# Kernel optimization log

Measured on AMD Instinct MI355X. Metric: run time of the kernel, lower is better.

## Reference

```python
import jax, jax.numpy as jnp
import numpy as np

B, C, H, W = 4, 8, 384, 384
CHANS = 18  # MLP hidden width (module default chans=18)
BAND = 32   # half-width of acquired low-frequency band


def setup_inputs() -> dict:
    key = jax.random.key(0)
    ks = jax.random.split(key, 8)
    acquired_kspace = jax.random.normal(ks[0], (B, C, H, W, 2), jnp.float32)
    acquiring_kspace = jax.random.normal(ks[1], (B, C, H, W, 2), jnp.float32)
    mid = W // 2
    am = np.zeros((B, W), np.float32)
    am[:, mid - BAND:mid + BAND] = 1.0  # acquired center band -> left/right well-defined
    acquired_mask = jnp.asarray(am)
    qm = np.zeros((B, W), np.float32)
    qm[:, ::24] = 1.0  # columns currently being acquired
    acquiring_mask = jnp.asarray(qm)
    CH = C * H
    IN = 2 * CH  # concat(acquiring_features, acquired_features)
    # MLP: Linear(IN,CHANS)+ReLU, Linear(CHANS,CHANS)+ReLU x2, Linear(CHANS,1)+Sigmoid (pools=4 layers)
    W1 = jax.random.normal(ks[2], (CHANS, IN), jnp.float32) * 0.02
    b1 = jnp.zeros((CHANS,), jnp.float32)
    W2 = jax.random.normal(ks[3], (CHANS, CHANS), jnp.float32) * 0.02
    b2 = jnp.zeros((CHANS,), jnp.float32)
    W3 = jax.random.normal(ks[4], (CHANS, CHANS), jnp.float32) * 0.02
    b3 = jnp.zeros((CHANS,), jnp.float32)
    W4 = jax.random.normal(ks[5], (1, CHANS), jnp.float32) * 0.02
    b4 = jnp.zeros((1,), jnp.float32)
    return dict(acquired_kspace=acquired_kspace, acquiring_kspace=acquiring_kspace,
                acquired_mask=acquired_mask, acquiring_mask=acquiring_mask,
                W1=W1, b1=b1, W2=W2, b2=b2, W3=W3, b3=b3, W4=W4, b4=b4)


def reference(acquired_kspace, acquiring_kspace, acquired_mask, acquiring_mask,
              W1, b1, W2, b2, W3, b3, W4, b4):
    cabs = lambda x: jnp.sqrt(jnp.sum(x * x, axis=-1))  # complex magnitude of trailing (re,im)
    # per-column flattened features, row-major over (C,H) like torch.flatten: [B, W, C*H]
    Fq = cabs(acquiring_kspace).transpose(0, 3, 1, 2).reshape(B, W, -1)
    Fa = cabs(acquired_kspace).transpose(0, 3, 1, 2).reshape(B, W, -1)
    CH = Fq.shape[-1]
    # split first linear over the concat([acquiring, acquired]) input
    Pq = Fq @ W1[:, :CH].T   # [B, W_i, CHANS]
    Pa = Fa @ W1[:, CH:].T   # [B, W_c, CHANS]
    h = jax.nn.relu(Pq[:, :, None, :] + Pa[:, None, :, :] + b1)  # [B, W_i, W_c, CHANS]
    h = jax.nn.relu(h @ W2.T + b2)
    h = jax.nn.relu(h @ W3.T + b3)
    out = jax.nn.sigmoid(h @ W4.T + b4)[..., 0]  # [B, W_i, W_c]
    # faithful left/right bounds from acquired_mask (same as torch.nonzero(...)[0][0])
    mid = W // 2
    right = mid + jnp.argmax(acquired_mask[:, mid:] < 1.0, axis=1)              # [B]
    left = jnp.argmax(acquired_mask[:, :mid][:, ::-1] < 1.0, axis=1) + 1        # [B]
    c = jnp.arange(W)
    cmask = (c[None, :] >= left[:, None]) & (c[None, :] < right[:, None])       # [B, W_c]
    denom = (right - left).astype(out.dtype)
    heat = jnp.sum(out * cmask[:, None, :].astype(out.dtype), axis=2) / denom[:, None]
    heat = jnp.where(acquiring_mask > 0, heat, jnp.zeros_like(heat))            # only nonzero acquiring cols
    return jnp.broadcast_to(heat[:, None, :], (B, H, W))  # torch.cat of h copies along dim=1
```

## Files before the change

### kernel.cpp

```cpp
#include <hip/hip_runtime.h>
#include <math.h>
#include <limits.h>

#define kB 4
#define kC 8
#define kH 384
#define kW 384
#define kCH (kC * kH)
#define kIN (2 * kCH)
#define kNC 18
#define kMID (kW / 2)

#define NCH 8
#define RPC (kCH / NCH)
#define NGRP 48
#define kN (kB * kW * kNC)

#define E18(M) M(0) M(1) M(2) M(3) M(4) M(5) M(6) M(7) M(8) M(9) M(10) M(11) M(12) M(13) M(14) M(15) M(16) M(17)
#define E12(M) M(0) M(1) M(2) M(3) M(4) M(5) M(6) M(7) M(8) M(9) M(10) M(11)

__device__ __forceinline__ void mask_wave0(const float* __restrict__ am, int b,
                                           int lane, int wave, int* sLR) {
    if (wave == 0) {
        int candR = INT_MAX, candL = INT_MAX;
#pragma unroll
        for (int k = 0; k < 3; ++k) {
            int i = lane + 64 * k;
            if (am[b * kW + kMID + i] < 1.0f) candR = min(candR, i);
            if (am[b * kW + (kMID - 1 - i)] < 1.0f) candL = min(candL, i);
        }
#pragma unroll
        for (int off = 32; off; off >>= 1) {
            candR = min(candR, __shfl_down(candR, off, 64));
            candL = min(candL, __shfl_down(candL, off, 64));
        }
        if (lane == 0) { sLR[0] = candL; sLR[1] = candR; }
    }
}

__global__ __launch_bounds__(256)
void proj_kernel(const float* __restrict__ acquired,
                 const float* __restrict__ acquiring,
                 const float* __restrict__ am,
                 const float* __restrict__ qm,
                 const float* __restrict__ W1,
                 float* __restrict__ Pq_part, float* __restrict__ Pa_part) {
    int g = blockIdx.x, chunk = blockIdx.y, b = blockIdx.z;
    int tid = threadIdx.x;
    int w0 = g * 8, r0 = chunk * RPC;
    int lane = tid & 63, wave = tid >> 6;

    __shared__ int sLR[2];
    __shared__ float sQm[8];
    mask_wave0(am, b, lane, wave, sLR);
    if (wave == 1 && lane < 8) sQm[lane] = qm[b * kW + w0 + lane];
    __syncthreads();
    int left  = ((sLR[0] == INT_MAX) ? 0 : sLR[0]) + 1;
    int right = kMID + ((sLR[1] == INT_MAX) ? 0 : sLR[1]);

    bool band = (left < w0 + 8) && (right > w0);
    bool acq_any = (sQm[0] > 0.f) || (sQm[1] > 0.f) || (sQm[2] > 0.f) || (sQm[3] > 0.f) ||
                   (sQm[4] > 0.f) || (sQm[5] > 0.f) || (sQm[6] > 0.f) || (sQm[7] > 0.f);
    if (!band && !acq_any) return;

    int c8 = tid & 7, r32 = tid >> 3;
    int w = w0 + c8;

    __shared__ float sW[RPC][20];
    __shared__ float sRed[4][8][kNC];

    for (int pass = 0; pass < 2; ++pass) {
        bool need = (pass == 0) ? band : acq_any;
        if (!need) continue;
        const float* ks = (pass == 0) ? acquired : acquiring;
        const float* w1 = (pass == 0) ? (W1 + kCH) : W1;

        const float* colp = ks + ((size_t)(b * kCH + r0 + r32) * kW + w) * 2;
#define KLOAD(it) const float2 v##it = *reinterpret_cast<const float2*>(colp + (size_t)(it) * 32 * kW * 2);
        E12(KLOAD)
#define KMAG(it) const float f##it = sqrtf(v##it.x * v##it.x + v##it.y * v##it.y);
        E12(KMAG)

        __syncthreads();
        for (int t = tid; t < kNC * RPC; t += 256) {
            int j = t / RPC, i = t - j * RPC;
            sW[i][j] = w1[j * kIN + r0 + i];
        }
        __syncthreads();

#define PDECL(j) float a##j = 0.0f;
        E18(PDECL)

#define ROWF(it) { \
            const float* row = &sW[r32 + 32 * (it)][0]; \
            const float4 q0 = *reinterpret_cast<const float4*>(row); \
            const float4 q1 = *reinterpret_cast<const float4*>(row + 4); \
            const float4 q2 = *reinterpret_cast<const float4*>(row + 8); \
            const float4 q3 = *reinterpret_cast<const float4*>(row + 12); \
            const float2 q4 = *reinterpret_cast<const float2*>(row + 16); \
            const float f = f##it; \
            a0  = fmaf(f, q0.x, a0);  a1  = fmaf(f, q0.y, a1);  \
            a2  = fmaf(f, q0.z, a2);  a3  = fmaf(f, q0.w, a3);  \
            a4  = fmaf(f, q1.x, a4);  a5  = fmaf(f, q1.y, a5);  \
            a6  = fmaf(f, q1.z, a6);  a7  = fmaf(f, q1.w, a7);  \
            a8  = fmaf(f, q2.x, a8);  a9  = fmaf(f, q2.y, a9);  \
            a10 = fmaf(f, q2.z, a10); a11 = fmaf(f, q2.w, a11); \
            a12 = fmaf(f, q3.x, a12); a13 = fmaf(f, q3.y, a13); \
            a14 = fmaf(f, q3.z, a14); a15 = fmaf(f, q3.w, a15); \
            a16 = fmaf(f, q4.x, a16); a17 = fmaf(f, q4.y, a17); }
        E12(ROWF)

#define WRED(j) { a##j += __shfl_down(a##j, 32, 64); a##j += __shfl_down(a##j, 16, 64); \
                  a##j += __shfl_down(a##j, 8, 64); }
        E18(WRED)
        if (lane < 8) {
#define SSTORE(j) sRed[wave][lane][j] = a##j;
            E18(SSTORE)
        }
        __syncthreads();
        if (tid < 8 * kNC) {
            int c = tid / kNC, j = tid - c * kNC;
            float s = sRed[0][c][j] + sRed[1][c][j] + sRed[2][c][j] + sRed[3][c][j];
            float* Pp = (pass == 0) ? Pa_part : Pq_part;
            Pp[((size_t)chunk * kB * kW + (size_t)b * kW + (w0 + c)) * kNC + j] = s;
        }
    }
}

__global__ __launch_bounds__(256)
void reduce_kernel(const float4* __restrict__ Pa_part, const float4* __restrict__ Pq_part,
                   float4* __restrict__ Pa, float4* __restrict__ Pq) {
    const int n4 = kN / 4;
    int idx = blockIdx.x * 256 + threadIdx.x;
    if (idx >= 2 * n4) return;
    const float4* src = (idx < n4) ? Pa_part : Pq_part;
    float4* dst = (idx < n4) ? Pa : Pq;
    int n = (idx < n4) ? idx : idx - n4;
    float4 s = make_float4(0.f, 0.f, 0.f, 0.f);
#pragma unroll
    for (int c = 0; c < NCH; ++c) {
        float4 v = src[(size_t)c * n4 + n];
        s.x += v.x; s.y += v.y; s.z += v.z; s.w += v.w;
    }
    dst[n] = s;
}

__global__ __launch_bounds__(256)
void pair_kernel(const float* __restrict__ Pq, const float* __restrict__ Pa,
                 const float* __restrict__ am, const float* __restrict__ qmask,
                 const float* __restrict__ b1, const float* __restrict__ W2,
                 const float* __restrict__ b2, const float* __restrict__ W3,
                 const float* __restrict__ b3, const float* __restrict__ W4,
                 const float* __restrict__ b4, float* __restrict__ heat) {
    int wi = blockIdx.x, b = blockIdx.y, tid = threadIdx.x;
    if (!(qmask[b * kW + wi] > 0.0f)) return;
    int lane = tid & 63, wave = tid >> 6;

    __shared__ int sLR[2];
    __shared__ float2 sW2[kNC * kNC / 2], sW3[kNC * kNC / 2];
    __shared__ float sW4[kNC], sb1[kNC], sb2[kNC], sb3[kNC], sPq[kNC];
    __shared__ float sb4s, wred[4];

    mask_wave0(am, b, lane, wave, sLR);
    if (tid >= 64 && tid < 64 + kNC * kNC / 2) {
        int t = tid - 64;
        sW2[t] = reinterpret_cast<const float2*>(W2)[t];
        sW3[t] = reinterpret_cast<const float2*>(W3)[t];
    }
    if (tid >= 224 && tid < 224 + kNC) {
        int j = tid - 224;
        sPq[j] = Pq[((size_t)(b * kW + wi)) * kNC + j];
        sW4[j] = W4[j]; sb1[j] = b1[j]; sb2[j] = b2[j]; sb3[j] = b3[j];
    }
    if (tid == 255) sb4s = b4[0];
    __syncthreads();

    int left  = ((sLR[0] == INT_MAX) ? 0 : sLR[0]) + 1;
    int right = kMID + ((sLR[1] == INT_MAX) ? 0 : sLR[1]);
    int span = right - left;

#define DOT2(S, k, v) (S[(k)*9+0].x*v##0  + S[(k)*9+0].y*v##1  + \
                       S[(k)*9+1].x*v##2  + S[(k)*9+1].y*v##3  + \
                       S[(k)*9+2].x*v##4  + S[(k)*9+2].y*v##5  + \
                       S[(k)*9+3].x*v##6  + S[(k)*9+3].y*v##7  + \
                       S[(k)*9+4].x*v##8  + S[(k)*9+4].y*v##9  + \
                       S[(k)*9+5].x*v##10 + S[(k)*9+5].y*v##11 + \
                       S[(k)*9+6].x*v##12 + S[(k)*9+6].y*v##13 + \
                       S[(k)*9+7].x*v##14 + S[(k)*9+7].y*v##15 + \
                       S[(k)*9+8].x*v##16 + S[(k)*9+8].y*v##17)

    float ssum = 0.0f;
    for (int wc = left + tid; wc < right; wc += 256) {
        const float* pa = Pa + (size_t)(b * kW + wc) * kNC;
#define L1(j) float x##j = fmaxf(sPq[j] + sb1[j] + pa[j], 0.0f);
        E18(L1)
        asm volatile("" ::: "memory");
#define L2(k) float y##k = fmaxf(sb2[k] + DOT2(sW2, k, x), 0.0f);
        E18(L2)
        asm volatile("" ::: "memory");
#define L3(k) float z##k = fmaxf(sb3[k] + DOT2(sW3, k, y), 0.0f);
        E18(L3)
        asm volatile("" ::: "memory");
        float t = sb4s +
            (sW4[0]*z0 + sW4[1]*z1 + sW4[2]*z2 + sW4[3]*z3 + sW4[4]*z4 + sW4[5]*z5 +
             sW4[6]*z6 + sW4[7]*z7 + sW4[8]*z8 + sW4[9]*z9 + sW4[10]*z10 + sW4[11]*z11 +
             sW4[12]*z12 + sW4[13]*z13 + sW4[14]*z14 + sW4[15]*z15 + sW4[16]*z16 + sW4[17]*z17);
        ssum += 1.0f / (1.0f + expf(-t));
    }

    ssum += __shfl_down(ssum, 32, 64); ssum += __shfl_down(ssum, 16, 64);
    ssum += __shfl_down(ssum,  8, 64); ssum += __shfl_down(ssum,  4, 64);
    ssum += __shfl_down(ssum,  2, 64); ssum += __shfl_down(ssum,  1, 64);
    if (lane == 0) wred[wave] = ssum;
    __syncthreads();
    if (tid == 0)
        heat[b * kW + wi] = (wred[0] + wred[1] + wred[2] + wred[3]) / (float)span;
}

__global__ __launch_bounds__(256)
void out_kernel(const float* __restrict__ heat, const float* __restrict__ qm,
                float4* __restrict__ out) {
    const int n4 = kB * kH * kW / 4;
    int idx = blockIdx.x * 256 + threadIdx.x;
    if (idx >= n4) return;
    int w4 = idx % (kW / 4);
    int b = idx / (kH * kW / 4);
    int base = b * kW + 4 * w4;
    float4 v;
    v.x = (qm[base + 0] > 0.0f) ? heat[base + 0] : 0.0f;
    v.y = (qm[base + 1] > 0.0f) ? heat[base + 1] : 0.0f;
    v.z = (qm[base + 2] > 0.0f) ? heat[base + 2] : 0.0f;
    v.w = (qm[base + 3] > 0.0f) ? heat[base + 3] : 0.0f;
    out[idx] = v;
}

extern "C" void kernel_launch(void* const* d_in, const int* in_sizes, int n_in,
                              void* d_out, int out_size, void* d_ws, size_t ws_size,
                              hipStream_t stream) {
    const float* acquired       = (const float*)d_in[0];
    const float* acquiring      = (const float*)d_in[1];
    const float* acquired_mask  = (const float*)d_in[2];
    const float* acquiring_mask = (const float*)d_in[3];
    const float* W1 = (const float*)d_in[4];
    const float* b1 = (const float*)d_in[5];
    const float* W2 = (const float*)d_in[6];
    const float* b2 = (const float*)d_in[7];
    const float* W3 = (const float*)d_in[8];
    const float* b3 = (const float*)d_in[9];
    const float* W4 = (const float*)d_in[10];
    const float* b4 = (const float*)d_in[11];
    float* out = (float*)d_out;

    float* Pa_part = (float*)d_ws;
    float* Pq_part = Pa_part + (size_t)NCH * kN;
    float* Pa      = Pq_part + (size_t)NCH * kN;
    float* Pq      = Pa + kN;
    float* heat    = Pq + kN;

    proj_kernel<<<dim3(NGRP, NCH, kB), 256, 0, stream>>>(
        acquired, acquiring, acquired_mask, acquiring_mask, W1, Pq_part, Pa_part);
    reduce_kernel<<<(2 * (kN / 4) + 255) / 256, 256, 0, stream>>>(
        (const float4*)Pa_part, (const float4*)Pq_part, (float4*)Pa, (float4*)Pq);
    pair_kernel<<<dim3(kW, kB), 256, 0, stream>>>(
        Pq, Pa, acquired_mask, acquiring_mask,
        b1, W2, b2, W3, b3, W4, b4, heat);
    out_kernel<<<(kB * kH * kW / 4 + 255) / 256, 256, 0, stream>>>(
        heat, acquiring_mask, (float4*)out);
}
```

Measured before the change: 149.4 us.

## Split projection passes into separate blocks, double row chunks, drop mask sync

The projection kernel now gives each of the two passes (acquired and acquiring) its own block through the z grid dimension, and doubles the number of row chunks, so every block loads 6 rows per thread instead of 12. The band/left-right mask search now runs in every wave with xor shuffles, and the acquiring-column check uses a wave ballot, which removes the shared-memory handoff and a barrier before the early exit. The aim is more parallel blocks and a shorter serial path per block for this memory-bound stage. The cost is twice as many partial buffers for the reduce kernel to sum, and W1 slices are reloaded in more blocks.

```diff
diff --git a/kernel.cpp b/kernel.cpp
--- a/kernel.cpp
+++ b/kernel.cpp
@@ -11,31 +11,30 @@
 #define kNC 18
 #define kMID (kW / 2)
 
-#define NCH 8
+#define NCH 16
 #define RPC (kCH / NCH)
 #define NGRP 48
 #define kN (kB * kW * kNC)
 
 #define E18(M) M(0) M(1) M(2) M(3) M(4) M(5) M(6) M(7) M(8) M(9) M(10) M(11) M(12) M(13) M(14) M(15) M(16) M(17)
-#define E12(M) M(0) M(1) M(2) M(3) M(4) M(5) M(6) M(7) M(8) M(9) M(10) M(11)
-
-__device__ __forceinline__ void mask_wave0(const float* __restrict__ am, int b,
-                                           int lane, int wave, int* sLR) {
-    if (wave == 0) {
-        int candR = INT_MAX, candL = INT_MAX;
+#define E6(M) M(0) M(1) M(2) M(3) M(4) M(5)
+
+__device__ __forceinline__ void mask_allwave(const float* __restrict__ am, int b,
+                                             int lane, int& left, int& right) {
+    int candR = INT_MAX, candL = INT_MAX;
 #pragma unroll
-        for (int k = 0; k < 3; ++k) {
-            int i = lane + 64 * k;
-            if (am[b * kW + kMID + i] < 1.0f) candR = min(candR, i);
-            if (am[b * kW + (kMID - 1 - i)] < 1.0f) candL = min(candL, i);
-        }
+    for (int k = 0; k < 3; ++k) {
+        int i = lane + 64 * k;
+        if (am[b * kW + kMID + i] < 1.0f) candR = min(candR, i);
+        if (am[b * kW + (kMID - 1 - i)] < 1.0f) candL = min(candL, i);
+    }
 #pragma unroll
-        for (int off = 32; off; off >>= 1) {
-            candR = min(candR, __shfl_down(candR, off, 64));
-            candL = min(candL, __shfl_down(candL, off, 64));
-        }
-        if (lane == 0) { sLR[0] = candL; sLR[1] = candR; }
-    }
+    for (int off = 1; off < 64; off <<= 1) {
+        candR = min(candR, __shfl_xor(candR, off, 64));
+        candL = min(candL, __shfl_xor(candL, off, 64));
+    }
+    left  = ((candL == INT_MAX) ? 0 : candL) + 1;
+    right = kMID + ((candR == INT_MAX) ? 0 : candR);
 }
 
 __global__ __launch_bounds__(256)
@@ -45,85 +44,76 @@
                  const float* __restrict__ qm,
                  const float* __restrict__ W1,
                  float* __restrict__ Pq_part, float* __restrict__ Pa_part) {
-    int g = blockIdx.x, chunk = blockIdx.y, b = blockIdx.z;
+    int g = blockIdx.x, chunk = blockIdx.y;
+    int b = blockIdx.z >> 1, pass = blockIdx.z & 1;
     int tid = threadIdx.x;
     int w0 = g * 8, r0 = chunk * RPC;
     int lane = tid & 63, wave = tid >> 6;
-
-    __shared__ int sLR[2];
-    __shared__ float sQm[8];
-    mask_wave0(am, b, lane, wave, sLR);
-    if (wave == 1 && lane < 8) sQm[lane] = qm[b * kW + w0 + lane];
-    __syncthreads();
-    int left  = ((sLR[0] == INT_MAX) ? 0 : sLR[0]) + 1;
-    int right = kMID + ((sLR[1] == INT_MAX) ? 0 : sLR[1]);
-
-    bool band = (left < w0 + 8) && (right > w0);
-    bool acq_any = (sQm[0] > 0.f) || (sQm[1] > 0.f) || (sQm[2] > 0.f) || (sQm[3] > 0.f) ||
-                   (sQm[4] > 0.f) || (sQm[5] > 0.f) || (sQm[6] > 0.f) || (sQm[7] > 0.f);
-    if (!band && !acq_any) return;
-
     int c8 = tid & 7, r32 = tid >> 3;
     int w = w0 + c8;
 
+    if (pass == 1) {
+        bool myq = qm[b * kW + w] > 0.0f;
+        if (__ballot(myq) == 0ULL) return;
+    } else {
+        int left, right;
+        mask_allwave(am, b, lane, left, right);
+        if (!((left < w0 + 8) && (right > w0))) return;
+    }
+
+    const float* ks = pass ? acquiring : acquired;
+    const float* w1 = pass ? W1 : (W1 + kCH);
+
+    const float* colp = ks + ((size_t)(b * kCH + r0 + r32) * kW + w) * 2;
+#define KLOAD(it) const float2 v##it = *reinterpret_cast<const float2*>(colp + (size_t)(it) * 32 * kW * 2);
+    E6(KLOAD)
+#define KMAG(it) const float f##it = sqrtf(v##it.x * v##it.x + v##it.y * v##it.y);
+    E6(KMAG)
+
     __shared__ float sW[RPC][20];
     __shared__ float sRed[4][8][kNC];
 
-    for (int pass = 0; pass < 2; ++pass) {
-        bool need = (pass == 0) ? band : acq_any;
-        if (!need) continue;
-        const float* ks = (pass == 0) ? acquired : acquiring;
-        const float* w1 = (pass == 0) ? (W1 + kCH) : W1;
-
-        const float* colp = ks + ((size_t)(b * kCH + r0 + r32) * kW + w) * 2;
-#define KLOAD(it) const float2 v##it = *reinterpret_cast<const float2*>(colp + (size_t)(it) * 32 * kW * 2);
-        E12(KLOAD)
-#define KMAG(it) const float f##it = sqrtf(v##it.x * v##it.x + v##it.y * v##it.y);
-        E12(KMAG)
-
-        __syncthreads();
-        for (int t = tid; t < kNC * RPC; t += 256) {
-            int j = t / RPC, i = t - j * RPC;
-            sW[i][j] = w1[j * kIN + r0 + i];
-        }
-        __syncthreads();
+    for (int t = tid; t < kNC * RPC; t += 256) {
+        int j = t / RPC, i = t - j * RPC;
+        sW[i][j] = w1[j * kIN + r0 + i];
+    }
+    __syncthreads();
 
 #define PDECL(j) float a##j = 0.0f;
-        E18(PDECL)
+    E18(PDECL)
 
 #define ROWF(it) { \
-            const float* row = &sW[r32 + 32 * (it)][0]; \
-            const float4 q0 = *reinterpret_cast<const float4*>(row); \
-            const float4 q1 = *reinterpret_cast<const float4*>(row + 4); \
-            const float4 q2 = *reinterpret_cast<const float4*>(row + 8); \
-            const float4 q3 = *reinterpret_cast<const float4*>(row + 12); \
-            const float2 q4 = *reinterpret_cast<const float2*>(row + 16); \
-            const float f = f##it; \
-            a0  = fmaf(f, q0.x, a0);  a1  = fmaf(f, q0.y, a1);  \
-            a2  = fmaf(f, q0.z, a2);  a3  = fmaf(f, q0.w, a3);  \
-            a4  = fmaf(f, q1.x, a4);  a5  = fmaf(f, q1.y, a5);  \
-            a6  = fmaf(f, q1.z, a6);  a7  = fmaf(f, q1.w, a7);  \
-            a8  = fmaf(f, q2.x, a8);  a9  = fmaf(f, q2.y, a9);  \
-            a10 = fmaf(f, q2.z, a10); a11 = fmaf(f, q2.w, a11); \
-            a12 = fmaf(f, q3.x, a12); a13 = fmaf(f, q3.y, a13); \
-            a14 = fmaf(f, q3.z, a14); a15 = fmaf(f, q3.w, a15); \
-            a16 = fmaf(f, q4.x, a16); a17 = fmaf(f, q4.y, a17); }
-        E12(ROWF)
+        const float* row = &sW[r32 + 32 * (it)][0]; \
+        const float4 q0 = *reinterpret_cast<const float4*>(row); \
+        const float4 q1 = *reinterpret_cast<const float4*>(row + 4); \
+        const float4 q2 = *reinterpret_cast<const float4*>(row + 8); \
+        const float4 q3 = *reinterpret_cast<const float4*>(row + 12); \
+        const float2 q4 = *reinterpret_cast<const float2*>(row + 16); \
+        const float f = f##it; \
+        a0  = fmaf(f, q0.x, a0);  a1  = fmaf(f, q0.y, a1);  \
+        a2  = fmaf(f, q0.z, a2);  a3  = fmaf(f, q0.w, a3);  \
+        a4  = fmaf(f, q1.x, a4);  a5  = fmaf(f, q1.y, a5);  \
+        a6  = fmaf(f, q1.z, a6);  a7  = fmaf(f, q1.w, a7);  \
+        a8  = fmaf(f, q2.x, a8);  a9  = fmaf(f, q2.y, a9);  \
+        a10 = fmaf(f, q2.z, a10); a11 = fmaf(f, q2.w, a11); \
+        a12 = fmaf(f, q3.x, a12); a13 = fmaf(f, q3.y, a13); \
+        a14 = fmaf(f, q3.z, a14); a15 = fmaf(f, q3.w, a15); \
+        a16 = fmaf(f, q4.x, a16); a17 = fmaf(f, q4.y, a17); }
+    E6(ROWF)
 
 #define WRED(j) { a##j += __shfl_down(a##j, 32, 64); a##j += __shfl_down(a##j, 16, 64); \
                   a##j += __shfl_down(a##j, 8, 64); }
-        E18(WRED)
-        if (lane < 8) {
+    E18(WRED)
+    if (lane < 8) {
 #define SSTORE(j) sRed[wave][lane][j] = a##j;
-            E18(SSTORE)
-        }
-        __syncthreads();
-        if (tid < 8 * kNC) {
-            int c = tid / kNC, j = tid - c * kNC;
-            float s = sRed[0][c][j] + sRed[1][c][j] + sRed[2][c][j] + sRed[3][c][j];
-            float* Pp = (pass == 0) ? Pa_part : Pq_part;
-            Pp[((size_t)chunk * kB * kW + (size_t)b * kW + (w0 + c)) * kNC + j] = s;
-        }
+        E18(SSTORE)
+    }
+    __syncthreads();
+    if (tid < 8 * kNC) {
+        int c = tid / kNC, j = tid - c * kNC;
+        float s = sRed[0][c][j] + sRed[1][c][j] + sRed[2][c][j] + sRed[3][c][j];
+        float* Pp = pass ? Pq_part : Pa_part;
+        Pp[((size_t)chunk * kB * kW + (size_t)b * kW + (w0 + c)) * kNC + j] = s;
     }
 }
 
@@ -156,16 +146,17 @@
     if (!(qmask[b * kW + wi] > 0.0f)) return;
     int lane = tid & 63, wave = tid >> 6;
 
-    __shared__ int sLR[2];
+    int left, right;
+    mask_allwave(am, b, lane, left, right);
+    int span = right - left;
+
     __shared__ float2 sW2[kNC * kNC / 2], sW3[kNC * kNC / 2];
     __shared__ float sW4[kNC], sb1[kNC], sb2[kNC], sb3[kNC], sPq[kNC];
     __shared__ float sb4s, wred[4];
 
-    mask_wave0(am, b, lane, wave, sLR);
-    if (tid >= 64 && tid < 64 + kNC * kNC / 2) {
-        int t = tid - 64;
-        sW2[t] = reinterpret_cast<const float2*>(W2)[t];
-        sW3[t] = reinterpret_cast<const float2*>(W3)[t];
+    if (tid < kNC * kNC / 2) {
+        sW2[tid] = reinterpret_cast<const float2*>(W2)[tid];
+        sW3[tid] = reinterpret_cast<const float2*>(W3)[tid];
     }
     if (tid >= 224 && tid < 224 + kNC) {
         int j = tid - 224;
@@ -174,10 +165,6 @@
     }
     if (tid == 255) sb4s = b4[0];
     __syncthreads();
-
-    int left  = ((sLR[0] == INT_MAX) ? 0 : sLR[0]) + 1;
-    int right = kMID + ((sLR[1] == INT_MAX) ? 0 : sLR[1]);
-    int span = right - left;
 
 #define DOT2(S, k, v) (S[(k)*9+0].x*v##0  + S[(k)*9+0].y*v##1  + \
                        S[(k)*9+1].x*v##2  + S[(k)*9+1].y*v##3  + \
@@ -257,7 +244,7 @@
     float* Pq      = Pa + kN;
     float* heat    = Pq + kN;
 
-    proj_kernel<<<dim3(NGRP, NCH, kB), 256, 0, stream>>>(
+    proj_kernel<<<dim3(NGRP, NCH, 2 * kB), 256, 0, stream>>>(
         acquired, acquiring, acquired_mask, acquiring_mask, W1, Pq_part, Pa_part);
     reduce_kernel<<<(2 * (kN / 4) + 255) / 256, 256, 0, stream>>>(
         (const float4*)Pa_part, (const float4*)Pq_part, (float4*)Pa, (float4*)Pq);
```

Result: no change. 150.3 us (+0.6%).
